# Kernel tuning notes

Hardware: AMD Instinct MI355X
Metric: run time of the kernel (lower is better)

## Reference

```python
import jax, jax.numpy as jnp
import numpy as np

DIM = 384
HEADS = 12
WIN = (2, 7, 7)
MLP_RATIO = 4.0
EPS = 1e-5


def _rel_index(Wt, Wh, Ww):
    t, h, w = np.meshgrid(np.arange(Wt), np.arange(Wh), np.arange(Ww), indexing='ij')
    coords = np.stack([t, h, w]).reshape(3, -1).T  # (N,3)
    rel = coords[:, None] - coords[None]  # (N,N,3)
    rel[..., 0] += Wt - 1
    rel[..., 1] += Wh - 1
    rel[..., 2] += Ww - 1
    rel[..., 0] *= (2 * Wh - 1) * (2 * Ww - 1)
    rel[..., 1] *= (2 * Ww - 1)
    return rel.sum(-1)  # (N,N) int


def setup_inputs() -> dict:
    key = jax.random.key(0)
    ks = jax.random.split(key, 16)
    d = DIM
    hdim = int(d * MLP_RATIO)
    Wt, Wh, Ww = WIN
    table_size = (2 * Wt - 1) * (2 * Wh - 1) * (2 * Ww - 1)
    s = lambda fan: 1.0 / np.sqrt(fan)
    return {
        'x': jax.random.normal(ks[0], (2, 8, 56, 56, d), jnp.float32),
        'norm1_g': jnp.ones((d,), jnp.float32),
        'norm1_b': jnp.zeros((d,), jnp.float32),
        'qkv_w': jax.random.normal(ks[1], (d, 3 * d), jnp.float32) * s(d),
        'qkv_b': jnp.zeros((3 * d,), jnp.float32),
        'proj_w': jax.random.normal(ks[2], (d, d), jnp.float32) * s(d),
        'proj_b': jnp.zeros((d,), jnp.float32),
        'bias_table': jax.random.normal(ks[3], (table_size, HEADS), jnp.float32) * 0.02,
        'norm2_g': jnp.ones((d,), jnp.float32),
        'norm2_b': jnp.zeros((d,), jnp.float32),
        'fc1_w': jax.random.normal(ks[4], (d, hdim), jnp.float32) * s(d),
        'fc1_b': jnp.zeros((hdim,), jnp.float32),
        'fc2_w': jax.random.normal(ks[5], (hdim, d), jnp.float32) * s(hdim),
        'fc2_b': jnp.zeros((d,), jnp.float32),
        'rel_index': jnp.asarray(_rel_index(*WIN), jnp.int32),
    }


def _ln(x, g, b):
    mu = x.mean(-1, keepdims=True)
    var = ((x - mu) ** 2).mean(-1, keepdims=True)
    return (x - mu) * jax.lax.rsqrt(var + EPS) * g + b


def _window_partition(x, win):
    B, T, H, W, C = x.shape
    Wt, Wh, Ww = win
    x = x.reshape(B, T // Wt, Wt, H // Wh, Wh, W // Ww, Ww, C)
    x = x.transpose(0, 1, 3, 5, 2, 4, 6, 7)
    return x.reshape(-1, Wt * Wh * Ww, C)


def _window_reverse(win_x, win, B, T, H, W):
    Wt, Wh, Ww = win
    C = win_x.shape[-1]
    x = win_x.reshape(B, T // Wt, H // Wh, W // Ww, Wt, Wh, Ww, C)
    x = x.transpose(0, 1, 4, 2, 5, 3, 6, 7)
    return x.reshape(B, T, H, W, C)


def reference(x, norm1_g, norm1_b, qkv_w, qkv_b, proj_w, proj_b, bias_table,
              norm2_g, norm2_b, fc1_w, fc1_b, fc2_w, fc2_b, rel_index):
    B, T, H, W, C = x.shape
    Wt, Wh, Ww = WIN
    N = Wt * Wh * Ww
    shift = (Wt // 2, Wh // 2, Ww // 2)
    head_dim = C // HEADS
    scale = head_dim ** -0.5

    shortcut = x
    h = _ln(x, norm1_g, norm1_b)
    h = jnp.roll(h, shift=(-shift[0], -shift[1], -shift[2]), axis=(1, 2, 3))
    # dims chosen divisible by window -> no padding branch
    wins = _window_partition(h, WIN)  # (BnW, N, C)
    BnW = wins.shape[0]

    qkv = wins @ qkv_w + qkv_b  # (BnW, N, 3C)
    qkv = qkv.reshape(BnW, N, 3, HEADS, head_dim).transpose(2, 0, 3, 1, 4)
    q, k, v = qkv[0] * scale, qkv[1], qkv[2]  # (BnW, H, N, d)

    bias = bias_table[rel_index.reshape(-1)].reshape(N, N, HEADS).transpose(2, 0, 1)
    attn = jnp.einsum('bhnd,bhmd->bhnm', q, k) + bias[None]
    attn = jax.nn.softmax(attn, axis=-1)
    out = jnp.einsum('bhnm,bhmd->bhnd', attn, v)
    out = out.transpose(0, 2, 1, 3).reshape(BnW, N, C)
    out = out @ proj_w + proj_b

    h = _window_reverse(out.reshape(-1, Wt, Wh, Ww, C), WIN, B, T, H, W)
    h = jnp.roll(h, shift=shift, axis=(1, 2, 3))
    x = shortcut + h

    h2 = _ln(x, norm2_g, norm2_b)
    h2 = jax.nn.gelu(h2 @ fc1_w + fc1_b, approximate=False) @ fc2_w + fc2_b
    return x + h2
```

## Files before the change

kernel.cpp:

```cpp
#include <hip/hip_runtime.h>
#include <cstdint>
#include <cstddef>


typedef __bf16 bf16x8 __attribute__((ext_vector_type(8)));
typedef __bf16 bf16x4 __attribute__((ext_vector_type(4)));
typedef float f32x4 __attribute__((ext_vector_type(4)));

#define DIM 384
#define QKV_DIM 1152
#define HID 1536
#define NHEADS 12
#define NTOK 50176
#define NWIN 512

__device__ __forceinline__ void gload16(const void* g, void* s) {
  __builtin_amdgcn_global_load_lds(
      (const __attribute__((address_space(1))) void*)g,
      (__attribute__((address_space(3))) void*)s, 16, 0, 0);
}

__global__ __launch_bounds__(256) void build_tokmap_k(int* __restrict__ map) {
  int t = blockIdx.x * 256 + threadIdx.x;
  if (t >= NTOK) return;
  int win = t / 98, n = t - win * 98;
  int b = win >> 8, tw = (win >> 6) & 3, hw = (win >> 3) & 7, ww = win & 7;
  int dt = n / 49; int rem = n - dt * 49; int dh = rem / 7, dw = rem - dh * 7;
  int t0 = (tw * 2 + dt + 1) & 7;
  int h0 = hw * 7 + dh + 3; if (h0 >= 56) h0 -= 56;
  int w0 = ww * 7 + dw + 3; if (w0 >= 56) w0 -= 56;
  map[t] = ((b * 8 + t0) * 56 + h0) * 56 + w0;
}

__global__ __launch_bounds__(256) void expand_biasp_k(const float* __restrict__ table,
                                                      const int* __restrict__ rel,
                                                      float* __restrict__ out) {
  int e = blockIdx.x * 256 + threadIdx.x;
  if (e >= NHEADS * 49 * 256) return;
  int r = e & 3, l = (e >> 2) & 63;
  int rest = e >> 8;
  int ni = rest % 7, mi = (rest / 7) % 7, h = rest / 49;
  int i = mi * 16 + (l >> 4) * 4 + r;
  int j = ni * 16 + (l & 15);
  float v;
  if (j >= 98) v = -1e30f;
  else if (i >= 98) v = 0.f;
  else v = table[rel[i * 98 + j] * NHEADS + h];
  out[e] = v;
}

__global__ __launch_bounds__(256) void pack_w_k(const float* __restrict__ W,
                                                __bf16* __restrict__ WP,
                                                int K, int N, int nk,
                                                int scaleCols, float scale) {
  int idx = blockIdx.x * 256 + threadIdx.x;
  if (idx >= (K * N) >> 3) return;
  int l = idx & 63, f = (idx >> 6) & 7, wc = (idx >> 9) & 1;
  int rest = idx >> 10, kt = rest % nk, bn = rest / nk;
  int n = f >> 1, kk = f & 1;
  int row = bn * 128 + wc * 64 + n * 16 + (l & 15);
  int k0 = kt * 64 + (kk * 4 + (l >> 4)) * 8;
  float sc = (row < scaleCols) ? scale : 1.0f;
  bf16x8 v;
  #pragma unroll
  for (int j = 0; j < 8; ++j)
    v[j] = (__bf16)(W[(size_t)(k0 + j) * N + row] * sc);
  *(bf16x8*)(WP + (size_t)idx * 8) = v;
}

__global__ __launch_bounds__(256) void scale_bias_k(const float* __restrict__ b,
                                                    float* __restrict__ out,
                                                    int n, int scaleCols, float scale) {
  int e = blockIdx.x * 256 + threadIdx.x;
  if (e >= n) return;
  out[e] = b[e] * (e < scaleCols ? scale : 1.0f);
}

__global__ __launch_bounds__(384) void vtrans_k(const __bf16* __restrict__ qkv,
                                                __bf16* __restrict__ vt) {
  int win = blockIdx.x, t = threadIdx.x;
  const __bf16* base = qkv + (size_t)win * 98 * QKV_DIM + 768 + t;
  __bf16* orow = vt + ((size_t)win * 384 + t) * 128;
  #pragma unroll
  for (int c = 0; c < 16; ++c) {
    bf16x8 pk;
    #pragma unroll
    for (int e2 = 0; e2 < 8; ++e2) {
      int tok = c * 8 + e2;
      pk[e2] = (tok < 98) ? base[(size_t)tok * QKV_DIM] : (__bf16)0.f;
    }
    *(bf16x8*)(orow + c * 8) = pk;
  }
}

template <typename T>
__global__ __launch_bounds__(256) void ln_k(const T* __restrict__ x,
                                            const float* __restrict__ g,
                                            const float* __restrict__ bta,
                                            __bf16* __restrict__ out,
                                            const int* __restrict__ map) {
  int w = threadIdx.x >> 6, l = threadIdx.x & 63;
  int tok = blockIdx.x * 4 + w;
  int src = map ? map[tok] : tok;
  const T* row = x + (size_t)src * DIM;
  float v[6]; float s = 0.f;
  #pragma unroll
  for (int j = 0; j < 6; ++j) { v[j] = (float)row[l + 64 * j]; s += v[j]; }
  #pragma unroll
  for (int m = 1; m < 64; m <<= 1) s += __shfl_xor(s, m, 64);
  float mu = s * (1.f / DIM);
  float var = 0.f;
  #pragma unroll
  for (int j = 0; j < 6; ++j) { float d = v[j] - mu; var += d * d; }
  #pragma unroll
  for (int m = 1; m < 64; m <<= 1) var += __shfl_xor(var, m, 64);
  float rs = rsqrtf(var * (1.f / DIM) + 1e-5f);
  __bf16* orow = out + (size_t)tok * DIM;
  #pragma unroll
  for (int j = 0; j < 6; ++j) {
    int c = l + 64 * j;
    orow[c] = (__bf16)((v[j] - mu) * rs * g[c] + bta[c]);
  }
}

template <int EPI>
__global__ __launch_bounds__(256, 2) void gemm_k(const __bf16* __restrict__ A,
                                                 const __bf16* __restrict__ WP,
                                                 const float* __restrict__ bias,
                                                 int M, int N, int K,
                                                 __bf16* __restrict__ outb,
                                                 float* __restrict__ outf,
                                                 const float* __restrict__ residf,
                                                 const __bf16* __restrict__ residb,
                                                 const int* __restrict__ tokmap) {
  __shared__ __align__(1024) char lds[32768];
  const int tid = threadIdx.x;
  const int l = tid & 63, w = tid >> 6;
  const int lr = l & 15, lg = l >> 4;
  const int ntile = N >> 7;
  const int nwg8 = gridDim.x >> 3;
  const int bid = (blockIdx.x & 7) * nwg8 + (blockIdx.x >> 3);
  const int bm = bid / ntile, bn = bid - bm * ntile;
  const int m0 = bm << 7, n0 = bn << 7;
  const int wr = w >> 1, wc = w & 1;
  const int srow = l >> 3;
  const int sch = (l & 7) ^ srow;
  const __bf16* pa = A + (size_t)(m0 + w * 32 + srow) * K + sch * 8;
  const int doff = w * 4096;
  const int nk = K >> 6;
  const __bf16* pB = WP + ((size_t)bn * nk * 2 + wc) * 4096 + l * 8;

#define LOADB(dst, ktl)                                        \
  {                                                            \
    const __bf16* p_ = pB + (size_t)(ktl) * 8192;              \
    _Pragma("unroll")                                          \
    for (int f_ = 0; f_ < 8; ++f_)                             \
      dst[f_] = *(const bf16x8*)(p_ + f_ * 512);               \
  }

  bf16x8 b0[8], b1[8];
  LOADB(b0, 0);
  #pragma unroll
  for (int i = 0; i < 4; ++i)
    gload16(pa + (size_t)(i * 8) * K, lds + doff + i * 1024);

  f32x4 acc[4][4] = {};

  auto iter = [&](int kt, bf16x8 (&bc)[8], bf16x8 (&bnx)[8]) {
    const char* cur = lds + ((kt & 1) << 14);
    if (kt + 1 < nk) {
      LOADB(bnx, kt + 1);
      char* nxt = lds + (((kt + 1) & 1) << 14);
      const size_t koff = (size_t)(kt + 1) << 6;
      #pragma unroll
      for (int i = 0; i < 4; ++i)
        gload16(pa + (size_t)(i * 8) * K + koff, nxt + doff + i * 1024);
      asm volatile("s_waitcnt vmcnt(12)" ::: "memory");
    } else {
      asm volatile("s_waitcnt vmcnt(0)" ::: "memory");
    }
    asm volatile("s_barrier" ::: "memory");
    #pragma unroll
    for (int kk = 0; kk < 2; ++kk) {
      bf16x8 af[4];
      const int ck = (kk << 2) + lg;
      #pragma unroll
      for (int m = 0; m < 4; ++m) {
        int r = (wr << 6) + (m << 4) + lr;
        af[m] = *(const bf16x8*)(cur + (r << 7) + ((ck ^ (r & 7)) << 4));
      }
      #pragma unroll
      for (int m = 0; m < 4; ++m)
        #pragma unroll
        for (int n = 0; n < 4; ++n)
          acc[m][n] = __builtin_amdgcn_mfma_f32_16x16x32_bf16(bc[n * 2 + kk], af[m],
                                                              acc[m][n], 0, 0, 0);
    }
    asm volatile("s_barrier" ::: "memory");
  };

  for (int kt = 0; kt < nk; kt += 2) {
    iter(kt, b0, b1);
    iter(kt + 1, b1, b0);
  }
#undef LOADB

  #pragma unroll
  for (int m = 0; m < 4; ++m) {
    const int grow = m0 + (wr << 6) + (m << 4) + lr;
    #pragma unroll
    for (int n = 0; n < 4; ++n) {
      const int gcol = n0 + (wc << 6) + (n << 4) + (lg << 2);
      f32x4 a = acc[m][n] + *(const f32x4*)(bias + gcol);
      if (EPI == 0) {
        bf16x4 c;
        #pragma unroll
        for (int r = 0; r < 4; ++r) c[r] = (__bf16)a[r];
        *(bf16x4*)(outb + (size_t)grow * N + gcol) = c;
      } else if (EPI == 1) {
        int dst = tokmap[grow];
        f32x4 rv = *(const f32x4*)(residf + (size_t)dst * DIM + gcol);
        bf16x4 c;
        #pragma unroll
        for (int r = 0; r < 4; ++r) c[r] = (__bf16)(rv[r] + a[r]);
        *(bf16x4*)(outb + (size_t)dst * DIM + gcol) = c;
      } else if (EPI == 2) {
        bf16x4 c;
        #pragma unroll
        for (int r = 0; r < 4; ++r) {
          float vv = a[r];
          float y = vv * (1.0f + 0.044715f * vv * vv);
          c[r] = (__bf16)(vv / (1.0f + __expf(-1.5957691216057308f * y)));
        }
        *(bf16x4*)(outb + (size_t)grow * N + gcol) = c;
      } else {
        bf16x4 sv = *(const bf16x4*)(residb + (size_t)grow * N + gcol);
        f32x4 o;
        #pragma unroll
        for (int r = 0; r < 4; ++r) o[r] = (float)sv[r] + a[r];
        *(f32x4*)(outf + (size_t)grow * N + gcol) = o;
      }
    }
  }
}

__global__ __launch_bounds__(64) void attn_k(const __bf16* __restrict__ qkv,
                                             const __bf16* __restrict__ vt,
                                             const float* __restrict__ pb,
                                             __bf16* __restrict__ out) {
  __shared__ __align__(1024) char P[4096];
  const int l = threadIdx.x, lr = l & 15, lg = l >> 4;
  const int bid = blockIdx.x;
  const int xc = bid & 7, kk = bid >> 3;
  const int wh = (kk / 7) * 8 + xc, mi = kk % 7;
  const int win = wh / NHEADS, h = wh - win * NHEADS;
  const size_t wbase = (size_t)win * 98 * QKV_DIM;
  const __bf16* qb = qkv + wbase + h * 32;
  const __bf16* kb = qb + 384;
  const bf16x8 z8 = {};
  const f32x4 fz = {};

  bf16x8 kf[7];
  #pragma unroll
  for (int ni = 0; ni < 7; ++ni) {
    int tok = ni * 16 + lr;
    kf[ni] = (tok < 98) ? *(const bf16x8*)(kb + (size_t)tok * QKV_DIM + lg * 8) : z8;
  }
  int qt = mi * 16 + lr;
  bf16x8 qf = (qt < 98) ? *(const bf16x8*)(qb + (size_t)qt * QKV_DIM + lg * 8) : z8;
  const f32x4* pbp = (const f32x4*)pb + (size_t)((h * 7 + mi) * 7) * 64 + l;
  f32x4 bv[7];
  #pragma unroll
  for (int ni = 0; ni < 7; ++ni) bv[ni] = pbp[ni * 64];

  f32x4 s[7];
  #pragma unroll
  for (int ni = 0; ni < 7; ++ni)
    s[ni] = __builtin_amdgcn_mfma_f32_16x16x32_bf16(qf, kf[ni], fz, 0, 0, 0);

  if (l < 32) {
    int row = l >> 1, c = 14 + (l & 1);
    *(f32x4*)(P + row * 256 + ((c ^ (row & 7)) << 4)) = fz;
  }

  #pragma unroll
  for (int r = 0; r < 4; ++r) {
    float mx = -1e30f;
    #pragma unroll
    for (int ni = 0; ni < 7; ++ni) {
      float vv = s[ni][r] + bv[ni][r];
      s[ni][r] = vv;
      mx = fmaxf(mx, vv);
    }
    #pragma unroll
    for (int m2 = 1; m2 < 16; m2 <<= 1) mx = fmaxf(mx, __shfl_xor(mx, m2, 64));
    float sum = 0.f;
    #pragma unroll
    for (int ni = 0; ni < 7; ++ni) { float p = __expf(s[ni][r] - mx); s[ni][r] = p; sum += p; }
    #pragma unroll
    for (int m2 = 1; m2 < 16; m2 <<= 1) sum += __shfl_xor(sum, m2, 64);
    float inv = 1.0f / sum;
    int il = lg * 4 + r;
    #pragma unroll
    for (int ni = 0; ni < 7; ++ni) {
      int j = ni * 16 + lr;
      *(__bf16*)(P + il * 256 + (((j >> 3) ^ (il & 7)) << 4) + ((j & 7) << 1)) =
          (__bf16)(s[ni][r] * inv);
    }
  }
  __syncthreads();

  bf16x8 pa[4];
  #pragma unroll
  for (int ks = 0; ks < 4; ++ks) {
    int ck = ks * 4 + lg;
    pa[ks] = *(const bf16x8*)(P + lr * 256 + ((ck ^ (lr & 7)) << 4));
  }
  const __bf16* vrow = vt + ((size_t)wh * 32) * 128;
  __bf16* ob = out + ((size_t)win * 98 + mi * 16) * DIM + h * 32;
  #pragma unroll
  for (int nf = 0; nf < 2; ++nf) {
    int d = nf * 16 + lr;
    f32x4 o = fz;
    #pragma unroll
    for (int ks = 0; ks < 4; ++ks) {
      bf16x8 vb = *(const bf16x8*)(vrow + (size_t)d * 128 + ks * 32 + lg * 8);
      o = __builtin_amdgcn_mfma_f32_16x16x32_bf16(pa[ks], vb, o, 0, 0, 0);
    }
    #pragma unroll
    for (int r = 0; r < 4; ++r) {
      int il = lg * 4 + r;
      if (mi * 16 + il < 98) ob[(size_t)il * DIM + nf * 16 + lr] = (__bf16)o[r];
    }
  }
}

extern "C" void kernel_launch(void* const* d_in, const int* in_sizes, int n_in,
                              void* d_out, int out_size, void* d_ws, size_t ws_size,
                              hipStream_t stream) {
  const float* x      = (const float*)d_in[0];
  const float* n1g    = (const float*)d_in[1];
  const float* n1b    = (const float*)d_in[2];
  const float* qkv_w  = (const float*)d_in[3];
  const float* qkv_b  = (const float*)d_in[4];
  const float* proj_w = (const float*)d_in[5];
  const float* proj_b = (const float*)d_in[6];
  const float* btab   = (const float*)d_in[7];
  const float* n2g    = (const float*)d_in[8];
  const float* n2b    = (const float*)d_in[9];
  const float* fc1_w  = (const float*)d_in[10];
  const float* fc1_b  = (const float*)d_in[11];
  const float* fc2_w  = (const float*)d_in[12];
  const float* fc2_b  = (const float*)d_in[13];
  const int*   relidx = (const int*)d_in[14];
  float* outp = (float*)d_out;
  (void)in_sizes; (void)n_in; (void)out_size; (void)ws_size;

  char* ws = (char*)d_ws;
  size_t off = 0;
  auto alloc = [&](size_t bytes) {
    char* p = ws + off;
    off = (off + bytes + 255) & ~(size_t)255;
    return p;
  };
  int*    tokmap = (int*)alloc((size_t)NTOK * 4);
  float*  biasex = (float*)alloc((size_t)NHEADS * 49 * 256 * 4);
  __bf16* wqkvP  = (__bf16*)alloc((size_t)QKV_DIM * DIM * 2);
  __bf16* wprojP = (__bf16*)alloc((size_t)DIM * DIM * 2);
  __bf16* wfc1P  = (__bf16*)alloc((size_t)HID * DIM * 2);
  __bf16* wfc2P  = (__bf16*)alloc((size_t)DIM * HID * 2);
  float*  qkvbS  = (float*)alloc((size_t)QKV_DIM * 4);
  __bf16* tokens = (__bf16*)alloc((size_t)NTOK * DIM * 2);
  __bf16* qkvbuf = (__bf16*)alloc((size_t)NTOK * HID * 2);
  __bf16* s1     = (__bf16*)alloc((size_t)NTOK * DIM * 2);
  __bf16* attnout = tokens;
  __bf16* h1 = qkvbuf;
  __bf16* vt = (__bf16*)d_out;

  const float scale = 0.17677669529663687f;

  build_tokmap_k<<<NTOK / 256, 256, 0, stream>>>(tokmap);
  expand_biasp_k<<<(NHEADS * 49 * 256) / 256, 256, 0, stream>>>(btab, relidx, biasex);
  pack_w_k<<<(DIM * QKV_DIM / 8) / 256, 256, 0, stream>>>(qkv_w, wqkvP, DIM, QKV_DIM, 6, DIM, scale);
  pack_w_k<<<(DIM * DIM / 8) / 256, 256, 0, stream>>>(proj_w, wprojP, DIM, DIM, 6, 0, 1.0f);
  pack_w_k<<<(DIM * HID / 8) / 256, 256, 0, stream>>>(fc1_w, wfc1P, DIM, HID, 6, 0, 1.0f);
  pack_w_k<<<(HID * DIM / 8) / 256, 256, 0, stream>>>(fc2_w, wfc2P, HID, DIM, 24, 0, 1.0f);
  scale_bias_k<<<(QKV_DIM + 255) / 256, 256, 0, stream>>>(qkv_b, qkvbS, QKV_DIM, DIM, scale);

  ln_k<float><<<NTOK / 4, 256, 0, stream>>>(x, n1g, n1b, tokens, tokmap);
  gemm_k<0><<<(NTOK / 128) * (QKV_DIM / 128), 256, 0, stream>>>(
      tokens, wqkvP, qkvbS, NTOK, QKV_DIM, DIM, qkvbuf, nullptr, nullptr, nullptr, nullptr);
  vtrans_k<<<NWIN, 384, 0, stream>>>(qkvbuf, vt);
  attn_k<<<NWIN * NHEADS * 7, 64, 0, stream>>>(qkvbuf, vt, biasex, attnout);
  gemm_k<1><<<(NTOK / 128) * (DIM / 128), 256, 0, stream>>>(
      attnout, wprojP, proj_b, NTOK, DIM, DIM, s1, nullptr, x, nullptr, tokmap);
  ln_k<__bf16><<<NTOK / 4, 256, 0, stream>>>(s1, n2g, n2b, tokens, nullptr);
  gemm_k<2><<<(NTOK / 128) * (HID / 128), 256, 0, stream>>>(
      tokens, wfc1P, fc1_b, NTOK, HID, DIM, h1, nullptr, nullptr, nullptr, nullptr);
  gemm_k<3><<<(NTOK / 128) * (DIM / 128), 256, 0, stream>>>(
      h1, wfc2P, fc2_b, NTOK, DIM, HID, nullptr, outp, nullptr, s1, nullptr);
}
```

Measured before the change: 504.8 us.

## Restructure GEMM to 256x64 tiles with per-wave private A staging

```diff
diff --git a/kernel.cpp b/kernel.cpp
--- a/kernel.cpp
+++ b/kernel.cpp
@@ -55,16 +55,16 @@
                                                 int scaleCols, float scale) {
   int idx = blockIdx.x * 256 + threadIdx.x;
   if (idx >= (K * N) >> 3) return;
-  int l = idx & 63, f = (idx >> 6) & 7, wc = (idx >> 9) & 1;
-  int rest = idx >> 10, kt = rest % nk, bn = rest / nk;
+  int l = idx & 63, f = (idx >> 6) & 7;
+  int rest = idx >> 9, kt = rest % nk, cn = rest / nk;
   int n = f >> 1, kk = f & 1;
-  int row = bn * 128 + wc * 64 + n * 16 + (l & 15);
+  int col = cn * 64 + n * 16 + (l & 15);
   int k0 = kt * 64 + (kk * 4 + (l >> 4)) * 8;
-  float sc = (row < scaleCols) ? scale : 1.0f;
+  float sc = (col < scaleCols) ? scale : 1.0f;
   bf16x8 v;
   #pragma unroll
   for (int j = 0; j < 8; ++j)
-    v[j] = (__bf16)(W[(size_t)(k0 + j) * N + row] * sc);
+    v[j] = (__bf16)(W[(size_t)(k0 + j) * N + col] * sc);
   *(bf16x8*)(WP + (size_t)idx * 8) = v;
 }
 
@@ -124,111 +124,117 @@
 }
 
 template <int EPI>
-__global__ __launch_bounds__(256, 2) void gemm_k(const __bf16* __restrict__ A,
-                                                 const __bf16* __restrict__ WP,
-                                                 const float* __restrict__ bias,
-                                                 int M, int N, int K,
-                                                 __bf16* __restrict__ outb,
-                                                 float* __restrict__ outf,
-                                                 const float* __restrict__ residf,
-                                                 const __bf16* __restrict__ residb,
-                                                 const int* __restrict__ tokmap) {
+__global__ __launch_bounds__(256) void gemm_k(const __bf16* __restrict__ A,
+                                              const __bf16* __restrict__ WP,
+                                              const float* __restrict__ bias,
+                                              int M, int N, int K,
+                                              __bf16* __restrict__ outb,
+                                              float* __restrict__ outf,
+                                              const float* __restrict__ residf,
+                                              const __bf16* __restrict__ residb,
+                                              const int* __restrict__ tokmap) {
   __shared__ __align__(1024) char lds[32768];
   const int tid = threadIdx.x;
   const int l = tid & 63, w = tid >> 6;
   const int lr = l & 15, lg = l >> 4;
-  const int ntile = N >> 7;
-  const int nwg8 = gridDim.x >> 3;
-  const int bid = (blockIdx.x & 7) * nwg8 + (blockIdx.x >> 3);
-  const int bm = bid / ntile, bn = bid - bm * ntile;
-  const int m0 = bm << 7, n0 = bn << 7;
-  const int wr = w >> 1, wc = w & 1;
-  const int srow = l >> 3;
-  const int sch = (l & 7) ^ srow;
-  const __bf16* pa = A + (size_t)(m0 + w * 32 + srow) * K + sch * 8;
-  const int doff = w * 4096;
+  const int ntile = N >> 6;
+  const int nwg = gridDim.x, qd = nwg >> 3, rm = nwg & 7;
+  const int xcd = blockIdx.x & 7;
+  const int wgid = (xcd < rm ? xcd * (qd + 1) : rm * (qd + 1) + (xcd - rm) * qd)
+                   + (blockIdx.x >> 3);
+  const int bm = wgid / ntile, bn = wgid - bm * ntile;
+  const int m0 = (bm << 8) + (w << 6);
+  const int n0 = bn << 6;
   const int nk = K >> 6;
-  const __bf16* pB = WP + ((size_t)bn * nk * 2 + wc) * 4096 + l * 8;
-
-#define LOADB(dst, ktl)                                        \
-  {                                                            \
-    const __bf16* p_ = pB + (size_t)(ktl) * 8192;              \
-    _Pragma("unroll")                                          \
-    for (int f_ = 0; f_ < 8; ++f_)                             \
-      dst[f_] = *(const bf16x8*)(p_ + f_ * 512);               \
-  }
-
-  bf16x8 b0[8], b1[8];
-  LOADB(b0, 0);
-  #pragma unroll
-  for (int i = 0; i < 4; ++i)
-    gload16(pa + (size_t)(i * 8) * K, lds + doff + i * 1024);
-
+  const int sch = (l & 7) ^ ((l >> 3) & 7);
+  const __bf16* pa = A + (size_t)(m0 + (l >> 3)) * K + sch * 8;
+  char* abuf = lds + (w << 13);
+  const __bf16* pB = WP + (size_t)bn * nk * 4096 + l * 8;
+
+#define STAGEA(kt)                                                   \
+  {                                                                  \
+    const size_t ko_ = (size_t)(kt) << 6;                            \
+    _Pragma("unroll")                                                \
+    for (int s_ = 0; s_ < 8; ++s_)                                   \
+      gload16(pa + (size_t)(s_ * 8) * K + ko_, abuf + s_ * 1024);    \
+  }
+#define LOADB(kt)                                                    \
+  {                                                                  \
+    const __bf16* p_ = pB + (size_t)(kt) * 4096;                     \
+    _Pragma("unroll")                                                \
+    for (int f_ = 0; f_ < 8; ++f_)                                   \
+      b[f_] = *(const bf16x8*)(p_ + f_ * 512);                       \
+  }
+#define LDA()                                                        \
+  {                                                                  \
+    _Pragma("unroll")                                                \
+    for (int kk_ = 0; kk_ < 2; ++kk_) {                              \
+      const int ck_ = (kk_ << 2) + lg;                               \
+      _Pragma("unroll")                                              \
+      for (int m_ = 0; m_ < 4; ++m_) {                               \
+        int r_ = (m_ << 4) + lr;                                     \
+        a[m_][kk_] = *(const bf16x8*)(abuf + (r_ << 7) +             \
+                                      ((ck_ ^ (r_ & 7)) << 4));      \
+      }                                                              \
+    }                                                                \
+    asm volatile("s_waitcnt lgkmcnt(0)" ::: "memory");               \
+    __builtin_amdgcn_sched_barrier(0);                               \
+  }
+
+  bf16x8 a[4][2], b[8];
   f32x4 acc[4][4] = {};
 
-  auto iter = [&](int kt, bf16x8 (&bc)[8], bf16x8 (&bnx)[8]) {
-    const char* cur = lds + ((kt & 1) << 14);
-    if (kt + 1 < nk) {
-      LOADB(bnx, kt + 1);
-      char* nxt = lds + (((kt + 1) & 1) << 14);
-      const size_t koff = (size_t)(kt + 1) << 6;
-      #pragma unroll
-      for (int i = 0; i < 4; ++i)
-        gload16(pa + (size_t)(i * 8) * K + koff, nxt + doff + i * 1024);
-      asm volatile("s_waitcnt vmcnt(12)" ::: "memory");
-    } else {
-      asm volatile("s_waitcnt vmcnt(0)" ::: "memory");
-    }
-    asm volatile("s_barrier" ::: "memory");
-    #pragma unroll
-    for (int kk = 0; kk < 2; ++kk) {
-      bf16x8 af[4];
-      const int ck = (kk << 2) + lg;
-      #pragma unroll
-      for (int m = 0; m < 4; ++m) {
-        int r = (wr << 6) + (m << 4) + lr;
-        af[m] = *(const bf16x8*)(cur + (r << 7) + ((ck ^ (r & 7)) << 4));
-      }
+  STAGEA(0)
+  asm volatile("s_waitcnt vmcnt(0)" ::: "memory");
+  LDA()
+
+  for (int kt = 0; kt < nk; ++kt) {
+    LOADB(kt)
+    const bool pf = (kt + 1 < nk);
+    if (pf) STAGEA(kt + 1)
+    __builtin_amdgcn_s_setprio(1);
+    #pragma unroll
+    for (int kk = 0; kk < 2; ++kk)
       #pragma unroll
       for (int m = 0; m < 4; ++m)
         #pragma unroll
         for (int n = 0; n < 4; ++n)
-          acc[m][n] = __builtin_amdgcn_mfma_f32_16x16x32_bf16(bc[n * 2 + kk], af[m],
+          acc[m][n] = __builtin_amdgcn_mfma_f32_16x16x32_bf16(b[n * 2 + kk], a[m][kk],
                                                               acc[m][n], 0, 0, 0);
-    }
-    asm volatile("s_barrier" ::: "memory");
-  };
-
-  for (int kt = 0; kt < nk; kt += 2) {
-    iter(kt, b0, b1);
-    iter(kt + 1, b1, b0);
-  }
+    __builtin_amdgcn_s_setprio(0);
+    if (pf) {
+      asm volatile("s_waitcnt vmcnt(0)" ::: "memory");
+      LDA()
+    }
+  }
+#undef STAGEA
 #undef LOADB
+#undef LDA
 
   #pragma unroll
   for (int m = 0; m < 4; ++m) {
-    const int grow = m0 + (wr << 6) + (m << 4) + lr;
+    const int grow = m0 + (m << 4) + lr;
     #pragma unroll
     for (int n = 0; n < 4; ++n) {
-      const int gcol = n0 + (wc << 6) + (n << 4) + (lg << 2);
-      f32x4 a = acc[m][n] + *(const f32x4*)(bias + gcol);
+      const int gcol = n0 + (n << 4) + (lg << 2);
+      f32x4 a4 = acc[m][n] + *(const f32x4*)(bias + gcol);
       if (EPI == 0) {
         bf16x4 c;
         #pragma unroll
-        for (int r = 0; r < 4; ++r) c[r] = (__bf16)a[r];
+        for (int r = 0; r < 4; ++r) c[r] = (__bf16)a4[r];
         *(bf16x4*)(outb + (size_t)grow * N + gcol) = c;
       } else if (EPI == 1) {
         int dst = tokmap[grow];
         f32x4 rv = *(const f32x4*)(residf + (size_t)dst * DIM + gcol);
         bf16x4 c;
         #pragma unroll
-        for (int r = 0; r < 4; ++r) c[r] = (__bf16)(rv[r] + a[r]);
+        for (int r = 0; r < 4; ++r) c[r] = (__bf16)(rv[r] + a4[r]);
         *(bf16x4*)(outb + (size_t)dst * DIM + gcol) = c;
       } else if (EPI == 2) {
         bf16x4 c;
         #pragma unroll
         for (int r = 0; r < 4; ++r) {
-          float vv = a[r];
+          float vv = a4[r];
           float y = vv * (1.0f + 0.044715f * vv * vv);
           c[r] = (__bf16)(vv / (1.0f + __expf(-1.5957691216057308f * y)));
         }
@@ -237,7 +243,7 @@
         bf16x4 sv = *(const bf16x4*)(residb + (size_t)grow * N + gcol);
         f32x4 o;
         #pragma unroll
-        for (int r = 0; r < 4; ++r) o[r] = (float)sv[r] + a[r];
+        for (int r = 0; r < 4; ++r) o[r] = (float)sv[r] + a4[r];
         *(f32x4*)(outf + (size_t)grow * N + gcol) = o;
       }
     }
@@ -388,15 +394,15 @@
   scale_bias_k<<<(QKV_DIM + 255) / 256, 256, 0, stream>>>(qkv_b, qkvbS, QKV_DIM, DIM, scale);
 
   ln_k<float><<<NTOK / 4, 256, 0, stream>>>(x, n1g, n1b, tokens, tokmap);
-  gemm_k<0><<<(NTOK / 128) * (QKV_DIM / 128), 256, 0, stream>>>(
+  gemm_k<0><<<(NTOK / 256) * (QKV_DIM / 64), 256, 0, stream>>>(
       tokens, wqkvP, qkvbS, NTOK, QKV_DIM, DIM, qkvbuf, nullptr, nullptr, nullptr, nullptr);
   vtrans_k<<<NWIN, 384, 0, stream>>>(qkvbuf, vt);
   attn_k<<<NWIN * NHEADS * 7, 64, 0, stream>>>(qkvbuf, vt, biasex, attnout);
-  gemm_k<1><<<(NTOK / 128) * (DIM / 128), 256, 0, stream>>>(
+  gemm_k<1><<<(NTOK / 256) * (DIM / 64), 256, 0, stream>>>(
       attnout, wprojP, proj_b, NTOK, DIM, DIM, s1, nullptr, x, nullptr, tokmap);
   ln_k<__bf16><<<NTOK / 4, 256, 0, stream>>>(s1, n2g, n2b, tokens, nullptr);
-  gemm_k<2><<<(NTOK / 128) * (HID / 128), 256, 0, stream>>>(
+  gemm_k<2><<<(NTOK / 256) * (HID / 64), 256, 0, stream>>>(
       tokens, wfc1P, fc1_b, NTOK, HID, DIM, h1, nullptr, nullptr, nullptr, nullptr);
-  gemm_k<3><<<(NTOK / 128) * (DIM / 128), 256, 0, stream>>>(
+  gemm_k<3><<<(NTOK / 256) * (DIM / 64), 256, 0, stream>>>(
       h1, wfc2P, fc2_b, NTOK, DIM, HID, nullptr, outp, nullptr, s1, nullptr);
 }
```

New measurement: 520.7 us. +3.2%, slower.
